# Optimization experiments

Measured on AMD Instinct MI355X. Metric: run time of the kernel, lower is better.

The kernel has to match this reference:

```python
import jax, jax.numpy as jnp
import numpy as np

B, S, C = 8, 2048, 1024
DROPOUT_RATE = 0.1


def setup_inputs() -> dict:
    key = jax.random.key(0)
    k1, k2, k3 = jax.random.split(key, 3)
    x = jax.random.normal(k1, (B, S, C), dtype=jnp.float32)
    # Fixed orthogonal projection buffer, as in __init__: U from SVD of a random matrix
    rand_mat = jax.random.normal(k2, (C, C), dtype=jnp.float32)
    U, _, _ = jnp.linalg.svd(rand_mat)
    U = U.astype(jnp.float32)
    # Base random permutation of [0, C)
    perm = jax.random.permutation(k3, C).astype(jnp.int32)
    # Stand-in for random.randint(0, 1000), fixed for determinism
    randint = 123
    return {"x": x, "U": U, "perm": perm, "randint": randint}


def reference(x, U, perm, randint):
    # channel_dim == -1, so the transpose in the original forward is a no-op.
    rand_scale = (DROPOUT_RATE / (1.0 - DROPOUT_RATE)) ** 0.5
    n = x.shape[-1]
    b = x.size // n
    # _randperm_like: per-row permutation ans[b_, i] = perm[i] * (6*randint*b_ + 1) mod n.
    # Reduce the multiplier mod n first so int32 arithmetic never overflows
    # (math is identical since (a*b) % n == (a*(b%n)) % n).
    batch_rand = (jnp.arange(b, dtype=jnp.int32) * (randint * 6) + 1) % n  # [b]
    ans = (perm[None, :] * batch_rand[:, None]) % n                        # [b, n]
    ans = ans.reshape(x.shape)                                             # same shape as x

    x_g = jnp.take_along_axis(x, ans, axis=-1)   # gather per-row permuted channels
    y = jnp.matmul(x_g, U)                        # shared (C,C) projection
    # scatter_(-1, ans, y) places y[..., j] at position ans[..., j]; since ans is a
    # permutation per row, this equals gathering y with the inverse permutation.
    inv = jnp.argsort(ans, axis=-1)
    x_next = jnp.take_along_axis(y, inv, axis=-1)
    return x_next * rand_scale + x
```

## Files before the change

kernel.cpp:

```cpp
#include <hip/hip_runtime.h>
#include <hip/hip_bf16.h>

#define WS_UT    ((size_t)0)
#define WS_XG    ((size_t)2*1024*1024)
#define WS_Y     ((size_t)34*1024*1024)

typedef __attribute__((ext_vector_type(8))) short short8;
typedef __attribute__((ext_vector_type(4))) float floatx4;

__device__ __forceinline__ void load_lds16(const void* g, void* l) {
  __builtin_amdgcn_global_load_lds(
      (const __attribute__((address_space(1))) void*)g,
      (__attribute__((address_space(3))) void*)l, 16, 0, 0);
}

__device__ __forceinline__ unsigned short f2bf(float f) {
  __hip_bfloat16 h = __float2bfloat16(f);
  return __builtin_bit_cast(unsigned short, h);
}
__device__ __forceinline__ float bf2f(unsigned short u) {
  return __uint_as_float(((unsigned)u) << 16);
}

__global__ void __launch_bounds__(256) prep_gather_k(const float* __restrict__ U,
                                                     const float* __restrict__ x,
                                                     const int* __restrict__ perm,
                                                     const int* __restrict__ prand,
                                                     unsigned short* __restrict__ ut,
                                                     unsigned short* __restrict__ xg) {
  __shared__ __align__(16) char smem[64 * 65 * 4];
  if (blockIdx.x < 256) {
    float (*tile)[65] = (float (*)[65])smem;
    const int tn = (blockIdx.x & 15) * 64;
    const int tk = (blockIdx.x >> 4) * 64;
    const int r = threadIdx.x >> 6;
    const int c = threadIdx.x & 63;
    for (int s = 0; s < 16; ++s)
      tile[s * 4 + r][c] = U[(size_t)(tk + s * 4 + r) * 1024 + tn + c];
    __syncthreads();
    for (int s = 0; s < 16; ++s)
      ut[(size_t)(tn + s * 4 + r) * 1024 + tk + c] = f2bf(tile[c][s * 4 + r]);
    return;
  }
  float (*xrow)[1024] = (float (*)[1024])smem;
  const int w = threadIdx.x >> 6, lane = threadIdx.x & 63;
  const int row = (blockIdx.x - 256) * 4 + w;
  const unsigned mult = ((unsigned)prand[0] * 6u) & 1023u;
  const unsigned br = (((unsigned)row & 1023u) * mult + 1u) & 1023u;
  const float* xr = x + (size_t)row * 1024;
  unsigned short* xo = xg + (size_t)row * 1024;
  for (int t = 0; t < 4; ++t) {
    floatx4 v = *(const floatx4*)(xr + t * 256 + lane * 4);
    *(floatx4*)(&xrow[w][t * 256 + lane * 4]) = v;
  }
  __syncthreads();
  for (int t = 0; t < 4; ++t) {
    int i0 = t * 256 + lane * 4;
    int4 p = *(const int4*)(perm + i0);
    ushort4 o;
    o.x = f2bf(xrow[w][((unsigned)p.x * br) & 1023u]);
    o.y = f2bf(xrow[w][((unsigned)p.y * br) & 1023u]);
    o.z = f2bf(xrow[w][((unsigned)p.z * br) & 1023u]);
    o.w = f2bf(xrow[w][((unsigned)p.w * br) & 1023u]);
    *(ushort4*)(xo + i0) = o;
  }
}

__global__ void __launch_bounds__(256, 2) gemm_k(const unsigned short* __restrict__ xg,
                                                 const unsigned short* __restrict__ ut,
                                                 unsigned short* __restrict__ y) {
  __shared__ __align__(16) char ldsA[32768];
  __shared__ __align__(16) char ldsB[16384];
  const int tid = threadIdx.x;
  const int w = tid >> 6, lane = tid & 63;
  const int l = blockIdx.x;
  const int xcd = l & 7;
  const int j = l >> 3;
  const int bn = (j & 7) * 128;
  const int bm = ((j >> 3) * 8 + xcd) * 256;
  const int wm = (w & 1) * 128, wn = (w >> 1) * 64;
  const int m = lane & 15, q = lane >> 4;
  const int srow = lane >> 3;
  const int sch = lane & 7;

  floatx4 acc[8][4];
  for (int i = 0; i < 8; ++i)
    for (int jj = 0; jj < 4; ++jj) acc[i][jj] = (floatx4)0.0f;

  for (int kt = 0; kt < 16; ++kt) {
    const int k0 = kt * 64;
    for (int t = 0; t < 8; ++t) {
      int row = w * 64 + t * 8 + srow;
      int sc = sch ^ (row & 7);
      load_lds16(xg + ((size_t)(bm + row) * 1024 + k0 + sc * 8),
                 ldsA + row * 128 + sch * 16);
    }
    for (int t = 0; t < 4; ++t) {
      int row = w * 32 + t * 8 + srow;
      int sc = sch ^ (row & 7);
      load_lds16(ut + ((size_t)(bn + row) * 1024 + k0 + sc * 8),
                 ldsB + row * 128 + sch * 16);
    }
    __syncthreads();
    for (int s = 0; s < 2; ++s) {
      short8 af[8], bfr[4];
      const int swz = ((s * 4 + q) ^ (m & 7)) * 16;
      for (int i = 0; i < 8; ++i)
        af[i] = *(const short8*)(ldsA + (wm + i * 16 + m) * 128 + swz);
      for (int jj = 0; jj < 4; ++jj)
        bfr[jj] = *(const short8*)(ldsB + (wn + jj * 16 + m) * 128 + swz);
      for (int i = 0; i < 8; ++i)
        for (int jj = 0; jj < 4; ++jj)
          acc[i][jj] = __builtin_amdgcn_mfma_f32_16x16x32_bf16(af[i], bfr[jj], acc[i][jj], 0, 0, 0);
    }
    __syncthreads();
  }
  for (int i = 0; i < 8; ++i) {
    int row = bm + wm + i * 16 + q * 4;
    for (int jj = 0; jj < 4; ++jj) {
      int col = bn + wn + jj * 16 + m;
      for (int r = 0; r < 4; ++r)
        y[(size_t)(row + r) * 1024 + col] = f2bf(acc[i][jj][r]);
    }
  }
}

__global__ void __launch_bounds__(256) scatter_out_k(const unsigned short* __restrict__ xg,
                                                     const unsigned short* __restrict__ y,
                                                     const int* __restrict__ perm,
                                                     const int* __restrict__ prand,
                                                     float* __restrict__ out) {
  __shared__ float obuf[4][1024];
  const int w = threadIdx.x >> 6, lane = threadIdx.x & 63;
  const int row = blockIdx.x * 4 + w;
  const unsigned mult = ((unsigned)prand[0] * 6u) & 1023u;
  const unsigned br = (((unsigned)row & 1023u) * mult + 1u) & 1023u;
  const unsigned short* yr = y + (size_t)row * 1024;
  const unsigned short* xr = xg + (size_t)row * 1024;
  for (int t = 0; t < 4; ++t) {
    int i0 = t * 256 + lane * 4;
    int4 p = *(const int4*)(perm + i0);
    ushort4 yv = *(const ushort4*)(yr + i0);
    ushort4 xv = *(const ushort4*)(xr + i0);
    obuf[w][((unsigned)p.x * br) & 1023u] = 0.3333333333333333f * bf2f(yv.x) + bf2f(xv.x);
    obuf[w][((unsigned)p.y * br) & 1023u] = 0.3333333333333333f * bf2f(yv.y) + bf2f(xv.y);
    obuf[w][((unsigned)p.z * br) & 1023u] = 0.3333333333333333f * bf2f(yv.z) + bf2f(xv.z);
    obuf[w][((unsigned)p.w * br) & 1023u] = 0.3333333333333333f * bf2f(yv.w) + bf2f(xv.w);
  }
  __syncthreads();
  float* orow = out + (size_t)row * 1024;
  for (int t = 0; t < 4; ++t) {
    int c0 = t * 256 + lane * 4;
    *(floatx4*)(orow + c0) = *(const floatx4*)(&obuf[w][c0]);
  }
}

extern "C" void kernel_launch(void* const* d_in, const int* in_sizes, int n_in,
                              void* d_out, int out_size, void* d_ws, size_t ws_size,
                              hipStream_t stream) {
  const float* x = (const float*)d_in[0];
  const float* U = (const float*)d_in[1];
  const int* perm = (const int*)d_in[2];
  const int* prand = (const int*)d_in[3];
  float* out = (float*)d_out;
  char* ws = (char*)d_ws;
  unsigned short* ut = (unsigned short*)(ws + WS_UT);
  unsigned short* xg = (unsigned short*)(ws + WS_XG);
  unsigned short* y = (unsigned short*)(ws + WS_Y);

  prep_gather_k<<<256 + 4096, 256, 0, stream>>>(U, x, perm, prand, ut, xg);
  gemm_k<<<512, 256, 0, stream>>>(xg, ut, y);
  scatter_out_k<<<4096, 256, 0, stream>>>(xg, y, perm, prand, out);
}
```

Before: 169.3 us.

## Fuse GEMM with inverse-permutation scatter and residual epilogue, full-row N tiles

Merges the GEMM and the scatter/residual kernel into one launch. Each block now owns 64 full rows across all 1024 output columns, so the inverse permutation can be applied in LDS and the scaled result plus residual written straight to the output. This drops the bf16 y round-trip and one launch. It also restructures the GEMM: A is double-buffered in LDS, B fragments are read directly from global memory and L2, and there are 512 threads and 256 blocks. The cost is fewer blocks and a large per-thread accumulator, which may reduce occupancy and lean heavily on L2 for B.

```diff
diff --git a/kernel.cpp b/kernel.cpp
--- a/kernel.cpp
+++ b/kernel.cpp
@@ -3,7 +3,6 @@
 
 #define WS_UT    ((size_t)0)
 #define WS_XG    ((size_t)2*1024*1024)
-#define WS_Y     ((size_t)34*1024*1024)
 
 typedef __attribute__((ext_vector_type(8))) short short8;
 typedef __attribute__((ext_vector_type(4))) float floatx4;
@@ -66,92 +65,105 @@
   }
 }
 
-__global__ void __launch_bounds__(256, 2) gemm_k(const unsigned short* __restrict__ xg,
-                                                 const unsigned short* __restrict__ ut,
-                                                 unsigned short* __restrict__ y) {
-  __shared__ __align__(16) char ldsA[32768];
-  __shared__ __align__(16) char ldsB[16384];
+__global__ void __launch_bounds__(512, 2) gemm_scatter_k(
+    const unsigned short* __restrict__ xg,
+    const unsigned short* __restrict__ ut,
+    const int* __restrict__ perm,
+    const int* __restrict__ prand,
+    float* __restrict__ out) {
+  __shared__ __align__(16) char smem[65536];
   const int tid = threadIdx.x;
   const int w = tid >> 6, lane = tid & 63;
-  const int l = blockIdx.x;
-  const int xcd = l & 7;
-  const int j = l >> 3;
-  const int bn = (j & 7) * 128;
-  const int bm = ((j >> 3) * 8 + xcd) * 256;
-  const int wm = (w & 1) * 128, wn = (w >> 1) * 64;
   const int m = lane & 15, q = lane >> 4;
-  const int srow = lane >> 3;
-  const int sch = lane & 7;
+  const int R0 = blockIdx.x * 64;
+  const int wn = w * 128;
 
-  floatx4 acc[8][4];
-  for (int i = 0; i < 8; ++i)
-    for (int jj = 0; jj < 4; ++jj) acc[i][jj] = (floatx4)0.0f;
+  const int x3 = m & 7;
+  const int qq = q ^ (x3 & 3);
+  const int sf = x3 >> 2;
+  const int offA0 = m * 128 + (qq + sf * 4) * 16;
+  const int offA1 = m * 128 + (qq + 4 - sf * 4) * 16;
 
+  const int sr = lane >> 3, sslot = lane & 7;
+  const unsigned short* asrc =
+      xg + (size_t)(R0 + w * 8 + sr) * 1024 + (size_t)((sslot ^ sr) * 8);
+  char* adst0 = smem + w * 1024 + lane * 16;
+
+  const unsigned short* bb[8];
+#pragma unroll
+  for (int jj = 0; jj < 8; ++jj)
+    bb[jj] = ut + (size_t)(wn + jj * 16 + m) * 1024 + q * 8;
+
+  floatx4 acc[4][8];
+#pragma unroll
+  for (int i = 0; i < 4; ++i)
+#pragma unroll
+    for (int jj = 0; jj < 8; ++jj) acc[i][jj] = (floatx4)0.0f;
+
+  load_lds16(asrc, adst0);
+  __syncthreads();
+
+#pragma unroll
   for (int kt = 0; kt < 16; ++kt) {
-    const int k0 = kt * 64;
-    for (int t = 0; t < 8; ++t) {
-      int row = w * 64 + t * 8 + srow;
-      int sc = sch ^ (row & 7);
-      load_lds16(xg + ((size_t)(bm + row) * 1024 + k0 + sc * 8),
-                 ldsA + row * 128 + sch * 16);
-    }
-    for (int t = 0; t < 4; ++t) {
-      int row = w * 32 + t * 8 + srow;
-      int sc = sch ^ (row & 7);
-      load_lds16(ut + ((size_t)(bn + row) * 1024 + k0 + sc * 8),
-                 ldsB + row * 128 + sch * 16);
+    const char* Ac = smem + (kt & 1) * 8192;
+    short8 b0[8];
+#pragma unroll
+    for (int jj = 0; jj < 8; ++jj)
+      b0[jj] = *(const short8*)(bb[jj] + kt * 64);
+    if (kt < 15)
+      load_lds16(asrc + (kt + 1) * 64, adst0 + ((kt + 1) & 1) * 8192);
+    short8 a0[4];
+#pragma unroll
+    for (int i = 0; i < 4; ++i) a0[i] = *(const short8*)(Ac + i * 2048 + offA0);
+    short8 b1[8];
+#pragma unroll
+    for (int jj = 0; jj < 8; ++jj)
+      b1[jj] = *(const short8*)(bb[jj] + kt * 64 + 32);
+#pragma unroll
+    for (int i = 0; i < 4; ++i)
+#pragma unroll
+      for (int jj = 0; jj < 8; ++jj)
+        acc[i][jj] = __builtin_amdgcn_mfma_f32_16x16x32_bf16(b0[jj], a0[i],
+                                                             acc[i][jj], 0, 0, 0);
+    short8 a1[4];
+#pragma unroll
+    for (int i = 0; i < 4; ++i) a1[i] = *(const short8*)(Ac + i * 2048 + offA1);
+#pragma unroll
+    for (int i = 0; i < 4; ++i)
+#pragma unroll
+      for (int jj = 0; jj < 8; ++jj)
+        acc[i][jj] = __builtin_amdgcn_mfma_f32_16x16x32_bf16(b1[jj], a1[i],
+                                                             acc[i][jj], 0, 0, 0);
+    __syncthreads();
+  }
+
+  const unsigned mult = ((unsigned)prand[0] * 6u) & 1023u;
+  const float rs = 0.33333334f;
+  float* sbuf = (float*)smem;
+#pragma unroll 1
+  for (int i = 0; i < 4; ++i) {
+    const int row = R0 + i * 16 + m;
+    const unsigned br = (((unsigned)row & 1023u) * mult + 1u) & 1023u;
+    const unsigned short* xr = xg + (size_t)row * 1024;
+#pragma unroll
+    for (int jj = 0; jj < 8; ++jj) {
+      const int j0 = wn + jj * 16 + q * 4;
+      const int4 p4 = *(const int4*)(perm + j0);
+      const ushort4 x4 = *(const ushort4*)(xr + j0);
+      sbuf[m * 1024 + (((unsigned)p4.x * br) & 1023u)] = rs * acc[i][jj][0] + bf2f(x4.x);
+      sbuf[m * 1024 + (((unsigned)p4.y * br) & 1023u)] = rs * acc[i][jj][1] + bf2f(x4.y);
+      sbuf[m * 1024 + (((unsigned)p4.z * br) & 1023u)] = rs * acc[i][jj][2] + bf2f(x4.z);
+      sbuf[m * 1024 + (((unsigned)p4.w * br) & 1023u)] = rs * acc[i][jj][3] + bf2f(x4.w);
     }
     __syncthreads();
-    for (int s = 0; s < 2; ++s) {
-      short8 af[8], bfr[4];
-      const int swz = ((s * 4 + q) ^ (m & 7)) * 16;
-      for (int i = 0; i < 8; ++i)
-        af[i] = *(const short8*)(ldsA + (wm + i * 16 + m) * 128 + swz);
-      for (int jj = 0; jj < 4; ++jj)
-        bfr[jj] = *(const short8*)(ldsB + (wn + jj * 16 + m) * 128 + swz);
-      for (int i = 0; i < 8; ++i)
-        for (int jj = 0; jj < 4; ++jj)
-          acc[i][jj] = __builtin_amdgcn_mfma_f32_16x16x32_bf16(af[i], bfr[jj], acc[i][jj], 0, 0, 0);
+    float* orow0 = out + (size_t)(R0 + i * 16) * 1024;
+#pragma unroll
+    for (int v = 0; v < 8; ++v) {
+      const int f = v * 512 + tid;
+      *(floatx4*)(orow0 + ((f >> 8) * 1024 + (f & 255) * 4)) =
+          *(const floatx4*)(sbuf + (size_t)f * 4);
     }
-    __syncthreads();
-  }
-  for (int i = 0; i < 8; ++i) {
-    int row = bm + wm + i * 16 + q * 4;
-    for (int jj = 0; jj < 4; ++jj) {
-      int col = bn + wn + jj * 16 + m;
-      for (int r = 0; r < 4; ++r)
-        y[(size_t)(row + r) * 1024 + col] = f2bf(acc[i][jj][r]);
-    }
-  }
-}
-
-__global__ void __launch_bounds__(256) scatter_out_k(const unsigned short* __restrict__ xg,
-                                                     const unsigned short* __restrict__ y,
-                                                     const int* __restrict__ perm,
-                                                     const int* __restrict__ prand,
-                                                     float* __restrict__ out) {
-  __shared__ float obuf[4][1024];
-  const int w = threadIdx.x >> 6, lane = threadIdx.x & 63;
-  const int row = blockIdx.x * 4 + w;
-  const unsigned mult = ((unsigned)prand[0] * 6u) & 1023u;
-  const unsigned br = (((unsigned)row & 1023u) * mult + 1u) & 1023u;
-  const unsigned short* yr = y + (size_t)row * 1024;
-  const unsigned short* xr = xg + (size_t)row * 1024;
-  for (int t = 0; t < 4; ++t) {
-    int i0 = t * 256 + lane * 4;
-    int4 p = *(const int4*)(perm + i0);
-    ushort4 yv = *(const ushort4*)(yr + i0);
-    ushort4 xv = *(const ushort4*)(xr + i0);
-    obuf[w][((unsigned)p.x * br) & 1023u] = 0.3333333333333333f * bf2f(yv.x) + bf2f(xv.x);
-    obuf[w][((unsigned)p.y * br) & 1023u] = 0.3333333333333333f * bf2f(yv.y) + bf2f(xv.y);
-    obuf[w][((unsigned)p.z * br) & 1023u] = 0.3333333333333333f * bf2f(yv.z) + bf2f(xv.z);
-    obuf[w][((unsigned)p.w * br) & 1023u] = 0.3333333333333333f * bf2f(yv.w) + bf2f(xv.w);
-  }
-  __syncthreads();
-  float* orow = out + (size_t)row * 1024;
-  for (int t = 0; t < 4; ++t) {
-    int c0 = t * 256 + lane * 4;
-    *(floatx4*)(orow + c0) = *(const floatx4*)(&obuf[w][c0]);
+    if (i < 3) __syncthreads();
   }
 }
 
@@ -166,9 +178,7 @@
   char* ws = (char*)d_ws;
   unsigned short* ut = (unsigned short*)(ws + WS_UT);
   unsigned short* xg = (unsigned short*)(ws + WS_XG);
-  unsigned short* y = (unsigned short*)(ws + WS_Y);
 
   prep_gather_k<<<256 + 4096, 256, 0, stream>>>(U, x, perm, prand, ut, xg);
-  gemm_k<<<512, 256, 0, stream>>>(xg, ut, y);
-  scatter_out_k<<<4096, 256, 0, stream>>>(xg, y, perm, prand, out);
+  gemm_scatter_k<<<256, 512, 0, stream>>>(xg, ut, perm, prand, out);
 }
```

Result: slower. 331.9 us (+96.0%).
